# Performance work log

Hardware: AMD Instinct MI355X
Metric: run time of the kernel (lower is better)

The kernel has to match this reference:

```python
import jax, jax.numpy as jnp
import numpy as np

B, DIM, H, W = 4, 256, 128, 128
ATTN_DIM, HEADS, WS = 64, 4, 5
HD = ATTN_DIM // HEADS
PAD = WS // 2
EPS = 1e-12


def setup_inputs() -> dict:
    key = jax.random.key(0)
    ks = jax.random.split(key, 6)
    return {
        "q_in": jax.random.normal(ks[0], (B, DIM, H, W), dtype=jnp.float32),
        "kv_in": jax.random.normal(ks[1], (B, DIM, H, W), dtype=jnp.float32),
        "Wq": jax.random.normal(ks[2], (ATTN_DIM, DIM), dtype=jnp.float32) * 0.05,
        "Wk": jax.random.normal(ks[3], (ATTN_DIM, DIM), dtype=jnp.float32) * 0.05,
        "Wv": jax.random.normal(ks[4], (ATTN_DIM, DIM), dtype=jnp.float32) * 0.05,
        "Wo": jax.random.normal(ks[5], (DIM, ATTN_DIM), dtype=jnp.float32) * 0.05,
    }


def _l2norm(x):
    return x / jnp.maximum(jnp.linalg.norm(x, axis=-1, keepdims=True), EPS)


def _unfold_windows(x, b, h, w):
    # x: (b, attn_dim, h, w) -> (b, heads, h*w, window_area, head_dim)
    # matches torch nn.Unfold ordering: channel-major, then kernel pos i*WS+j
    xp = jnp.pad(x, ((0, 0), (0, 0), (PAD, PAD), (PAD, PAD)), mode="reflect")
    patches = jnp.stack(
        [xp[:, :, i:i + h, j:j + w] for i in range(WS) for j in range(WS)],
        axis=2,
    )  # (b, attn_dim, WS*WS, h, w)
    patches = patches.reshape(b, HEADS, HD, WS * WS, h * w)
    return patches.transpose(0, 1, 4, 3, 2)  # (b, heads, hw, wa, hd)


def reference(q_in, kv_in, Wq, Wk, Wv, Wo):
    b, _, h, w = q_in.shape
    hw = h * w
    # 1x1 convs (no bias) as channel contractions
    q = jnp.einsum("oc,bchw->bohw", Wq, q_in)
    k = jnp.einsum("oc,bchw->bohw", Wk, kv_in)
    v = jnp.einsum("oc,bchw->bohw", Wv, kv_in)

    q = q.reshape(b, HEADS, HD, hw).transpose(0, 1, 3, 2)  # (b, heads, hw, hd)
    q = _l2norm(q)

    k = _l2norm(_unfold_windows(k, b, h, w))  # (b, heads, hw, wa, hd)
    v = _unfold_windows(v, b, h, w)

    # cosine attention over each local window (note: module never applies self.scale)
    attn = jnp.einsum("bnqd,bnqwd->bnqw", q, k)
    attn = jax.nn.softmax(attn, axis=-1)
    out = jnp.einsum("bnqw,bnqwd->bnqd", attn, v)  # (b, heads, hw, hd)

    out = out.transpose(0, 1, 3, 2).reshape(b, ATTN_DIM, h, w)
    return jnp.einsum("oc,bchw->bohw", Wo, out)
```

## Files before the change

### kernel.cpp

```cpp
#include <hip/hip_runtime.h>
#include <hip/hip_bf16.h>
#include <math.h>

#define B_ 4
#define DIM_ 256
#define H_ 128
#define W_ 128
#define HW_ (H_ * W_)
#define AD_ 64
#define HEADS_ 4
#define HD_ 16
#define WS_ 5
#define PAD_ 2

typedef __attribute__((ext_vector_type(8))) short short8;
typedef __attribute__((ext_vector_type(4))) float f32x4;
typedef __attribute__((ext_vector_type(4))) unsigned int u32x4;

__device__ __forceinline__ ushort f2bf(float f) {
    unsigned u = __builtin_bit_cast(unsigned, f);
    unsigned r = u + 0x7FFFu + ((u >> 16) & 1u);
    return (ushort)(r >> 16);
}
__device__ __forceinline__ float bf2f(ushort h) {
    return __builtin_bit_cast(float, (unsigned)h << 16);
}

__device__ __forceinline__ void splitpair(float x0, float x1,
                                          unsigned& hp, unsigned& lp) {
    unsigned u0 = __builtin_bit_cast(unsigned, x0);
    unsigned u1 = __builtin_bit_cast(unsigned, x1);
    hp = __builtin_amdgcn_perm(u1, u0, 0x07060302u);
    float r0 = x0 - __builtin_bit_cast(float, u0 & 0xFFFF0000u);
    float r1 = x1 - __builtin_bit_cast(float, u1 & 0xFFFF0000u);
    lp = __builtin_amdgcn_perm(__builtin_bit_cast(unsigned, r1),
                               __builtin_bit_cast(unsigned, r0), 0x07060302u);
}

__device__ __forceinline__ void gl16(const void* g, void* l) {
    __builtin_amdgcn_global_load_lds(
        (const __attribute__((address_space(1))) unsigned int*)g,
        (__attribute__((address_space(3))) unsigned int*)l, 16, 0, 0);
}

__global__ __launch_bounds__(256) void k_prep(
    const float* __restrict__ Wq, const float* __restrict__ Wk,
    const float* __restrict__ Wv, const float* __restrict__ Wo,
    ushort* __restrict__ WfQh, ushort* __restrict__ WfQl,
    ushort* __restrict__ WfKVh, ushort* __restrict__ WfKVl,
    ushort* __restrict__ WoFh, ushort* __restrict__ WoFl)
{
    int i = blockIdx.x * 256 + threadIdx.x;
    if (i < 16384) {
        int j = i & 7, l = (i >> 3) & 63, kc = (i >> 9) & 7, mt = i >> 12;
        int o = mt * 16 + (l & 15);
        int c = kc * 32 + ((l >> 4) & 3) * 8 + j;
        float wv = Wq[o * DIM_ + c];
        ushort h = f2bf(wv);
        WfQh[i] = h;
        WfQl[i] = f2bf(wv - bf2f(h));
        int kco = (i >> 9) & 1, mtg = i >> 10;
        int oo = mtg * 16 + (l & 15);
        int co = kco * 32 + ((l >> 4) & 3) * 8 + j;
        float wo = Wo[oo * AD_ + co];
        ushort ho = f2bf(wo);
        WoFh[i] = ho;
        WoFl[i] = f2bf(wo - bf2f(ho));
    } else if (i < 49152) {
        int ii = i - 16384;
        int j = ii & 7, l = (ii >> 3) & 63, kc = (ii >> 9) & 7, mt = ii >> 12;
        const float* Ws = (mt < 4) ? Wk : Wv;
        int o = (mt & 3) * 16 + (l & 15);
        int c = kc * 32 + ((l >> 4) & 3) * 8 + j;
        float wv = Ws[o * DIM_ + c];
        ushort h = f2bf(wv);
        WfKVh[ii] = h;
        WfKVl[ii] = f2bf(wv - bf2f(h));
    }
}

__device__ __forceinline__ void conv_b(const float* Xw, int lr, int kg,
                                       short8* bh, short8* bl)
{
#pragma unroll
    for (int nt = 0; nt < 2; ++nt) {
        u32x4 h, l;
#pragma unroll
        for (int jp = 0; jp < 4; ++jp) {
            float x0 = Xw[(kg * 8 + 2 * jp    ) * 32 + nt * 16 + lr];
            float x1 = Xw[(kg * 8 + 2 * jp + 1) * 32 + nt * 16 + lr];
            unsigned hp, lp;
            splitpair(x0, x1, hp, lp);
            h[jp] = hp;
            l[jp] = lp;
        }
        bh[nt] = __builtin_bit_cast(short8, h);
        bl[nt] = __builtin_bit_cast(short8, l);
    }
}

__global__ __launch_bounds__(256, 3) void k_qkv(
    const float* __restrict__ q_in, const float* __restrict__ kv_in,
    const ushort* __restrict__ WfQh, const ushort* __restrict__ WfQl,
    const ushort* __restrict__ WfKVh, const ushort* __restrict__ WfKVl,
    float* __restrict__ qh, float* __restrict__ kh, float* __restrict__ vv)
{
    __shared__ float Xl[3][4][32 * 32];

    int bid  = blockIdx.x;
    int g    = bid / 3;
    int role = bid - g * 3;
    int b    = g >> 7;
    int p0   = (g & 127) * 128;

    const float*  xsrc = (role == 0) ? q_in : kv_in;
    const ushort* Wh = (role == 0) ? WfQh : (role == 1) ? WfKVh : (WfKVh + 16384);
    const ushort* Wl = (role == 0) ? WfQl : (role == 1) ? WfKVl : (WfKVl + 16384);
    float* outp = (role == 0) ? qh : (role == 1) ? kh : vv;
    bool norm = (role < 2);

    int tid  = threadIdx.x;
    int lane = tid & 63;
    int wid  = __builtin_amdgcn_readfirstlane(tid >> 6);
    int lr = lane & 15, kg = lane >> 4;

    const float* xw = xsrc + ((size_t)b * DIM_ << 14) + p0 + wid * 32;

    short8 ah[2][4], al[2][4];

#pragma unroll
    for (int i = 0; i < 4; ++i) {
        int s = i * 64 + lane;
        gl16(xw + (size_t)(s >> 3) * HW_ + (s & 7) * 4, &Xl[0][wid][s * 4]);
    }
#pragma unroll
    for (int mt = 0; mt < 4; ++mt) {
        int off = (((mt * 8 + 0) << 6) + lane) * 8;
        ah[0][mt] = *(const short8*)(Wh + off);
        al[0][mt] = *(const short8*)(Wl + off);
    }
#pragma unroll
    for (int i = 0; i < 4; ++i) {
        int s = i * 64 + lane;
        gl16(xw + (size_t)(32 + (s >> 3)) * HW_ + (s & 7) * 4, &Xl[1][wid][s * 4]);
    }

    f32x4 acc[4][2];
#pragma unroll
    for (int mt = 0; mt < 4; ++mt)
#pragma unroll
        for (int nt = 0; nt < 2; ++nt) {
            f32x4 z = {0.f, 0.f, 0.f, 0.f};
            acc[mt][nt] = z;
        }

#pragma unroll
    for (int kc = 0; kc < 8; ++kc) {
        const int cs = kc & 1, ns = cs ^ 1;

        if (kc < 7) {
#pragma unroll
            for (int mt = 0; mt < 4; ++mt) {
                int off = (((mt * 8 + kc + 1) << 6) + lane) * 8;
                ah[ns][mt] = *(const short8*)(Wh + off);
                al[ns][mt] = *(const short8*)(Wl + off);
            }
        }
        if (kc < 6) {
#pragma unroll
            for (int i = 0; i < 4; ++i) {
                int s = i * 64 + lane;
                gl16(xw + (size_t)((kc + 2) * 32 + (s >> 3)) * HW_ + (s & 7) * 4,
                     &Xl[(kc + 2) % 3][wid][s * 4]);
            }
        }

        if (kc < 6)       asm volatile("s_waitcnt vmcnt(16)" ::: "memory");
        else if (kc == 6) asm volatile("s_waitcnt vmcnt(12)" ::: "memory");
        else              asm volatile("s_waitcnt vmcnt(0)"  ::: "memory");
        __builtin_amdgcn_sched_barrier(0);

        short8 bh[2], bl[2];
        conv_b(&Xl[kc % 3][wid][0], lr, kg, bh, bl);
#pragma unroll
        for (int mt = 0; mt < 4; ++mt) {
#pragma unroll
            for (int nt = 0; nt < 2; ++nt) {
                acc[mt][nt] = __builtin_amdgcn_mfma_f32_16x16x32_bf16(ah[cs][mt], bh[nt], acc[mt][nt], 0, 0, 0);
                acc[mt][nt] = __builtin_amdgcn_mfma_f32_16x16x32_bf16(ah[cs][mt], bl[nt], acc[mt][nt], 0, 0, 0);
                acc[mt][nt] = __builtin_amdgcn_mfma_f32_16x16x32_bf16(al[cs][mt], bh[nt], acc[mt][nt], 0, 0, 0);
            }
        }
    }

    int pr = p0 + wid * 32;
#pragma unroll
    for (int mt = 0; mt < 4; ++mt) {
#pragma unroll
        for (int nt = 0; nt < 2; ++nt) {
            f32x4 v = acc[mt][nt];
            if (norm) {
                float s = v.x * v.x + v.y * v.y + v.z * v.z + v.w * v.w;
                s += __shfl_xor(s, 16);
                s += __shfl_xor(s, 32);
                float inv = 1.f / fmaxf(sqrtf(s), 1e-12f);
                v.x *= inv; v.y *= inv; v.z *= inv; v.w *= inv;
            }
            float* dst = outp
                + (((size_t)(b * HEADS_ + mt) << 14) + pr + nt * 16 + lr) * HD_ + kg * 4;
            *(f32x4*)dst = v;
        }
    }
}

__device__ __forceinline__ int refl(int i, int n) {
    if (i < 0) i = -i;
    if (i >= n) i = 2 * n - 2 - i;
    return i;
}

__global__ __launch_bounds__(256) void k_attn(
    const float* __restrict__ qh, const float* __restrict__ kh,
    const float* __restrict__ vv, float* __restrict__ ao)
{
    int bid = blockIdx.x;
    int swz = (bid & 7) * 256 + (bid >> 3);
    int tid = threadIdx.x;
    int lane = tid & 63;
    int wv  = tid >> 6;
    int t   = lane >> 5;
    int pl  = lane & 31;

    int pix = swz * 128 + wv * 32 + pl;
    int p  = pix & (HW_ - 1);
    int bh = pix >> 14;
    int y = p >> 7, x = p & (W_ - 1);
    int to = t * 8;

    const float* qp = qh + ((size_t)bh * HW_ + p) * HD_ + to;
    float4 qa = *(const float4*)(qp + 0);
    float4 qb = *(const float4*)(qp + 4);

    float logit[WS_ * WS_];
    int   nidx [WS_ * WS_];
#pragma unroll
    for (int i = 0; i < WS_; ++i) {
        int ry = refl(y + i - PAD_, H_);
#pragma unroll
        for (int j = 0; j < WS_; ++j) {
            int rx = refl(x + j - PAD_, W_);
            int np_ = ry * W_ + rx;
            nidx[i*WS_ + j] = np_;
            const float* kp = kh + ((size_t)bh * HW_ + np_) * HD_ + to;
            float4 ka = *(const float4*)(kp + 0);
            float4 kb = *(const float4*)(kp + 4);
            float d = 0.f;
            d = fmaf(qa.x, ka.x, d); d = fmaf(qa.y, ka.y, d);
            d = fmaf(qa.z, ka.z, d); d = fmaf(qa.w, ka.w, d);
            d = fmaf(qb.x, kb.x, d); d = fmaf(qb.y, kb.y, d);
            d = fmaf(qb.z, kb.z, d); d = fmaf(qb.w, kb.w, d);
            logit[i*WS_ + j] = d + __shfl_xor(d, 32);
        }
    }

    float m = logit[0];
#pragma unroll
    for (int w = 1; w < WS_*WS_; ++w) m = fmaxf(m, logit[w]);
    float s = 0.f;
#pragma unroll
    for (int w = 0; w < WS_*WS_; ++w) { float e = expf(logit[w] - m); logit[w] = e; s += e; }
    float invs = 1.f / s;

    float a[8];
#pragma unroll
    for (int d = 0; d < 8; ++d) a[d] = 0.f;
#pragma unroll
    for (int w = 0; w < WS_*WS_; ++w) {
        float wt = logit[w] * invs;
        const float* vp = vv + ((size_t)bh * HW_ + nidx[w]) * HD_ + to;
        float4 va = *(const float4*)(vp + 0);
        float4 vb = *(const float4*)(vp + 4);
        a[0] = fmaf(wt, va.x, a[0]); a[1] = fmaf(wt, va.y, a[1]);
        a[2] = fmaf(wt, va.z, a[2]); a[3] = fmaf(wt, va.w, a[3]);
        a[4] = fmaf(wt, vb.x, a[4]); a[5] = fmaf(wt, vb.y, a[5]);
        a[6] = fmaf(wt, vb.z, a[6]); a[7] = fmaf(wt, vb.w, a[7]);
    }

    int b = bh >> 2, h = bh & 3;
    float* aop = ao + ((size_t)b * HW_ + p) * AD_ + h * HD_ + to;
    *(float4*)(aop + 0) = make_float4(a[0], a[1], a[2], a[3]);
    *(float4*)(aop + 4) = make_float4(a[4], a[5], a[6], a[7]);
}

__global__ __launch_bounds__(256) void k_oproj(
    const float* __restrict__ ao, const ushort* __restrict__ WoFh,
    const ushort* __restrict__ WoFl, float* __restrict__ out)
{
    int tid  = threadIdx.x;
    int lane = tid & 63;
    int wid  = __builtin_amdgcn_readfirstlane(tid >> 6);
    int lr = lane & 15, kg = lane >> 4;
    int pix = blockIdx.x * 16 + lr;
    int b = pix >> 14;
    int p = pix & (HW_ - 1);

    f32x4 acc[4];
#pragma unroll
    for (int mt = 0; mt < 4; ++mt) { f32x4 z = {0.f,0.f,0.f,0.f}; acc[mt] = z; }

#pragma unroll
    for (int kc = 0; kc < 2; ++kc) {
        const float* bp = ao + (size_t)pix * AD_ + kc * 32 + kg * 8;
        float4 x0 = *(const float4*)(bp + 0);
        float4 x1 = *(const float4*)(bp + 4);
        float xv[8] = {x0.x, x0.y, x0.z, x0.w, x1.x, x1.y, x1.z, x1.w};
        u32x4 hh, ll;
#pragma unroll
        for (int jp = 0; jp < 4; ++jp) {
            unsigned hp, lp;
            splitpair(xv[2 * jp], xv[2 * jp + 1], hp, lp);
            hh[jp] = hp;
            ll[jp] = lp;
        }
        short8 bh = __builtin_bit_cast(short8, hh);
        short8 bl = __builtin_bit_cast(short8, ll);
#pragma unroll
        for (int mt = 0; mt < 4; ++mt) {
            int mtg = wid * 4 + mt;
            short8 ah = *(const short8*)(WoFh + (((mtg * 2 + kc) << 6) + lane) * 8);
            short8 al = *(const short8*)(WoFl + (((mtg * 2 + kc) << 6) + lane) * 8);
            acc[mt] = __builtin_amdgcn_mfma_f32_16x16x32_bf16(ah, bh, acc[mt], 0, 0, 0);
            acc[mt] = __builtin_amdgcn_mfma_f32_16x16x32_bf16(ah, bl, acc[mt], 0, 0, 0);
            acc[mt] = __builtin_amdgcn_mfma_f32_16x16x32_bf16(al, bh, acc[mt], 0, 0, 0);
        }
    }

#pragma unroll
    for (int mt = 0; mt < 4; ++mt) {
        int oc = wid * 64 + mt * 16 + kg * 4;
        float* op = out + (size_t)b * DIM_ * HW_ + (size_t)oc * HW_ + p;
        op[0 * HW_] = acc[mt].x;
        op[1 * HW_] = acc[mt].y;
        op[2 * HW_] = acc[mt].z;
        op[3 * HW_] = acc[mt].w;
    }
}

extern "C" void kernel_launch(void* const* d_in, const int* in_sizes, int n_in,
                              void* d_out, int out_size, void* d_ws, size_t ws_size,
                              hipStream_t stream) {
    const float* q_in  = (const float*)d_in[0];
    const float* kv_in = (const float*)d_in[1];
    const float* Wq    = (const float*)d_in[2];
    const float* Wk    = (const float*)d_in[3];
    const float* Wv    = (const float*)d_in[4];
    const float* Wo    = (const float*)d_in[5];
    float* out = (float*)d_out;

    float* wsf = (float*)d_ws;
    ushort* u     = (ushort*)wsf;
    ushort* WfQh  = u;
    ushort* WfQl  = u + 16384;
    ushort* WfKVh = u + 32768;
    ushort* WfKVl = u + 65536;
    ushort* WoFh  = u + 98304;
    ushort* WoFl  = u + 114688;
    size_t tens = (size_t)B_ * HEADS_ * HW_ * HD_;
    float* qh = wsf + 65536;
    float* kh = qh + tens;
    float* vv = kh + tens;
    float* ao = vv + tens;

    k_prep<<<dim3(192), dim3(256), 0, stream>>>(Wq, Wk, Wv, Wo,
                                                WfQh, WfQl, WfKVh, WfKVl, WoFh, WoFl);
    k_qkv<<<dim3(1536), dim3(256), 0, stream>>>(q_in, kv_in,
                                                WfQh, WfQl, WfKVh, WfKVl, qh, kh, vv);
    k_attn <<<dim3(2048), dim3(256), 0, stream>>>(qh, kh, vv, ao);
    k_oproj<<<dim3(4096), dim3(256), 0, stream>>>(ao, WoFh, WoFl, out);
}
```

Baseline: 120.9 us.

## Fuse output projection into attention kernel via shared-memory staging

The attention kernel now has each block handle 32 pixels across all 4 heads, one head per wave. It stages the 32x64 attention output in LDS and then applies the Wo projection with split-bf16 MFMA directly, writing the final output. This removes the separate o-proj launch and the global round trip of the intermediate attention tensor. In exchange it adds a block barrier and LDS traffic, changes the pixel mapping and locality of the attention loads, and each block still reloads the Wo fragments.

Result: faster. 105.3 us (-12.9%).

```diff
diff --git a/kernel.cpp b/kernel.cpp
--- a/kernel.cpp
+++ b/kernel.cpp
@@ -221,19 +221,23 @@
 
 __global__ __launch_bounds__(256) void k_attn(
     const float* __restrict__ qh, const float* __restrict__ kh,
-    const float* __restrict__ vv, float* __restrict__ ao)
+    const float* __restrict__ vv, const ushort* __restrict__ WoFh,
+    const ushort* __restrict__ WoFl, float* __restrict__ out)
 {
+    __shared__ float aoL[32][65];
+
     int bid = blockIdx.x;
     int swz = (bid & 7) * 256 + (bid >> 3);
+    int b   = swz >> 9;
+    int p0  = (swz & 511) * 32;
     int tid = threadIdx.x;
     int lane = tid & 63;
-    int wv  = tid >> 6;
+    int w   = __builtin_amdgcn_readfirstlane(tid >> 6);
     int t   = lane >> 5;
     int pl  = lane & 31;
 
-    int pix = swz * 128 + wv * 32 + pl;
-    int p  = pix & (HW_ - 1);
-    int bh = pix >> 14;
+    int p  = p0 + pl;
+    int bh = b * HEADS_ + w;
     int y = p >> 7, x = p & (W_ - 1);
     int to = t * 8;
 
@@ -265,19 +269,19 @@
 
     float m = logit[0];
 #pragma unroll
-    for (int w = 1; w < WS_*WS_; ++w) m = fmaxf(m, logit[w]);
+    for (int q = 1; q < WS_*WS_; ++q) m = fmaxf(m, logit[q]);
     float s = 0.f;
 #pragma unroll
-    for (int w = 0; w < WS_*WS_; ++w) { float e = expf(logit[w] - m); logit[w] = e; s += e; }
+    for (int q = 0; q < WS_*WS_; ++q) { float e = expf(logit[q] - m); logit[q] = e; s += e; }
     float invs = 1.f / s;
 
     float a[8];
 #pragma unroll
     for (int d = 0; d < 8; ++d) a[d] = 0.f;
 #pragma unroll
-    for (int w = 0; w < WS_*WS_; ++w) {
-        float wt = logit[w] * invs;
-        const float* vp = vv + ((size_t)bh * HW_ + nidx[w]) * HD_ + to;
+    for (int q = 0; q < WS_*WS_; ++q) {
+        float wt = logit[q] * invs;
+        const float* vp = vv + ((size_t)bh * HW_ + nidx[q]) * HD_ + to;
         float4 va = *(const float4*)(vp + 0);
         float4 vb = *(const float4*)(vp + 4);
         a[0] = fmaf(wt, va.x, a[0]); a[1] = fmaf(wt, va.y, a[1]);
@@ -286,63 +290,66 @@
         a[6] = fmaf(wt, vb.z, a[6]); a[7] = fmaf(wt, vb.w, a[7]);
     }
 
-    int b = bh >> 2, h = bh & 3;
-    float* aop = ao + ((size_t)b * HW_ + p) * AD_ + h * HD_ + to;
-    *(float4*)(aop + 0) = make_float4(a[0], a[1], a[2], a[3]);
-    *(float4*)(aop + 4) = make_float4(a[4], a[5], a[6], a[7]);
-}
-
-__global__ __launch_bounds__(256) void k_oproj(
-    const float* __restrict__ ao, const ushort* __restrict__ WoFh,
-    const ushort* __restrict__ WoFl, float* __restrict__ out)
-{
-    int tid  = threadIdx.x;
-    int lane = tid & 63;
-    int wid  = __builtin_amdgcn_readfirstlane(tid >> 6);
+#pragma unroll
+    for (int j = 0; j < 8; ++j)
+        aoL[pl][w * HD_ + to + j] = a[j];
+    __syncthreads();
+
     int lr = lane & 15, kg = lane >> 4;
-    int pix = blockIdx.x * 16 + lr;
-    int b = pix >> 14;
-    int p = pix & (HW_ - 1);
-
-    f32x4 acc[4];
-#pragma unroll
-    for (int mt = 0; mt < 4; ++mt) { f32x4 z = {0.f,0.f,0.f,0.f}; acc[mt] = z; }
+
+    f32x4 acc[4][2];
+#pragma unroll
+    for (int mt = 0; mt < 4; ++mt)
+#pragma unroll
+        for (int nt = 0; nt < 2; ++nt) {
+            f32x4 z = {0.f, 0.f, 0.f, 0.f};
+            acc[mt][nt] = z;
+        }
 
 #pragma unroll
     for (int kc = 0; kc < 2; ++kc) {
-        const float* bp = ao + (size_t)pix * AD_ + kc * 32 + kg * 8;
-        float4 x0 = *(const float4*)(bp + 0);
-        float4 x1 = *(const float4*)(bp + 4);
-        float xv[8] = {x0.x, x0.y, x0.z, x0.w, x1.x, x1.y, x1.z, x1.w};
-        u32x4 hh, ll;
-#pragma unroll
-        for (int jp = 0; jp < 4; ++jp) {
-            unsigned hp, lp;
-            splitpair(xv[2 * jp], xv[2 * jp + 1], hp, lp);
-            hh[jp] = hp;
-            ll[jp] = lp;
-        }
-        short8 bh = __builtin_bit_cast(short8, hh);
-        short8 bl = __builtin_bit_cast(short8, ll);
+        short8 bh8[2], bl8[2];
+#pragma unroll
+        for (int nt = 0; nt < 2; ++nt) {
+            u32x4 hh, ll;
+#pragma unroll
+            for (int jp = 0; jp < 4; ++jp) {
+                float x0 = aoL[nt * 16 + lr][kc * 32 + kg * 8 + 2 * jp];
+                float x1 = aoL[nt * 16 + lr][kc * 32 + kg * 8 + 2 * jp + 1];
+                unsigned hp, lp;
+                splitpair(x0, x1, hp, lp);
+                hh[jp] = hp;
+                ll[jp] = lp;
+            }
+            bh8[nt] = __builtin_bit_cast(short8, hh);
+            bl8[nt] = __builtin_bit_cast(short8, ll);
+        }
 #pragma unroll
         for (int mt = 0; mt < 4; ++mt) {
-            int mtg = wid * 4 + mt;
+            int mtg = w * 4 + mt;
             short8 ah = *(const short8*)(WoFh + (((mtg * 2 + kc) << 6) + lane) * 8);
             short8 al = *(const short8*)(WoFl + (((mtg * 2 + kc) << 6) + lane) * 8);
-            acc[mt] = __builtin_amdgcn_mfma_f32_16x16x32_bf16(ah, bh, acc[mt], 0, 0, 0);
-            acc[mt] = __builtin_amdgcn_mfma_f32_16x16x32_bf16(ah, bl, acc[mt], 0, 0, 0);
-            acc[mt] = __builtin_amdgcn_mfma_f32_16x16x32_bf16(al, bh, acc[mt], 0, 0, 0);
+#pragma unroll
+            for (int nt = 0; nt < 2; ++nt) {
+                acc[mt][nt] = __builtin_amdgcn_mfma_f32_16x16x32_bf16(ah, bh8[nt], acc[mt][nt], 0, 0, 0);
+                acc[mt][nt] = __builtin_amdgcn_mfma_f32_16x16x32_bf16(ah, bl8[nt], acc[mt][nt], 0, 0, 0);
+                acc[mt][nt] = __builtin_amdgcn_mfma_f32_16x16x32_bf16(al, bh8[nt], acc[mt][nt], 0, 0, 0);
+            }
         }
     }
 
 #pragma unroll
     for (int mt = 0; mt < 4; ++mt) {
-        int oc = wid * 64 + mt * 16 + kg * 4;
-        float* op = out + (size_t)b * DIM_ * HW_ + (size_t)oc * HW_ + p;
-        op[0 * HW_] = acc[mt].x;
-        op[1 * HW_] = acc[mt].y;
-        op[2 * HW_] = acc[mt].z;
-        op[3 * HW_] = acc[mt].w;
+#pragma unroll
+        for (int nt = 0; nt < 2; ++nt) {
+            int oc = w * 64 + mt * 16 + kg * 4;
+            int px = p0 + nt * 16 + lr;
+            float* op = out + (size_t)b * DIM_ * HW_ + (size_t)oc * HW_ + px;
+            op[0 * HW_] = acc[mt][nt].x;
+            op[1 * HW_] = acc[mt][nt].y;
+            op[2 * HW_] = acc[mt][nt].z;
+            op[3 * HW_] = acc[mt][nt].w;
+        }
     }
 }
 
@@ -369,12 +376,10 @@
     float* qh = wsf + 65536;
     float* kh = qh + tens;
     float* vv = kh + tens;
-    float* ao = vv + tens;
 
     k_prep<<<dim3(192), dim3(256), 0, stream>>>(Wq, Wk, Wv, Wo,
                                                 WfQh, WfQl, WfKVh, WfKVl, WoFh, WoFl);
     k_qkv<<<dim3(1536), dim3(256), 0, stream>>>(q_in, kv_in,
                                                 WfQh, WfQl, WfKVh, WfKVl, qh, kh, vv);
-    k_attn <<<dim3(2048), dim3(256), 0, stream>>>(qh, kh, vv, ao);
-    k_oproj<<<dim3(4096), dim3(256), 0, stream>>>(ao, WoFh, WoFl, out);
-}
+    k_attn<<<dim3(2048), dim3(256), 0, stream>>>(qh, kh, vv, WoFh, WoFl, out);
+}
```
